# Kernel tuning notes

Measured on AMD Instinct MI355X. Metric: run time of the kernel, lower is better.

Reference implementation:

```python
import jax, jax.numpy as jnp
import numpy as np

B, S, DM = 2, 2048, 1024
H, HD = 16, 64  # heads, head_dims = dims // heads
SCALE = HD ** -0.5


def softmax_one(x):
    # softmax with +1 in the denominator: exp(x_i) / (1 + sum_j exp(x_j))
    # stable form: shift by m = max(max(x), 0)
    m = jnp.maximum(jnp.max(x, axis=-1, keepdims=True), 0.0)
    e = jnp.exp(x - m)
    return e / (jnp.exp(-m) + jnp.sum(e, axis=-1, keepdims=True))


def setup_inputs() -> dict:
    key = jax.random.key(0)
    ks = jax.random.split(key, 11)
    init = lambda k, shape, fan_in: jax.random.uniform(k, shape, jnp.float32, -1.0, 1.0) * (fan_in ** -0.5)
    return {
        "query": jax.random.normal(ks[0], (B, S, DM), jnp.float32),
        "key": jax.random.normal(ks[1], (B, S, DM), jnp.float32),
        "value": jax.random.normal(ks[2], (B, S, DM), jnp.float32),
        "Wq": init(ks[3], (H * HD, DM), DM), "bq": init(ks[4], (H * HD,), DM),
        "Wk": init(ks[5], (H * HD, DM), DM), "bk": init(ks[6], (H * HD,), DM),
        "Wv": init(ks[7], (H * HD, DM), DM), "bv": init(ks[8], (H * HD,), DM),
        "Wo": init(ks[9], (DM, H * HD), H * HD), "bo": init(ks[10], (DM,), H * HD),
    }


def _proj(x, W, b):
    # [B,S,DM] -> [B,H,S,HD]
    y = x @ W.T + b
    return y.reshape(B, S, H, HD).transpose(0, 2, 1, 3)


def reference(query, key, value, Wq, bq, Wk, bk, Wv, bv, Wo, bo):
    Q = _proj(query, Wq, bq)
    K = _proj(key, Wk, bk)
    V = _proj(value, Wv, bv)
    scores = jnp.einsum("bhqd,bhkd->bhqk", Q, K) * SCALE  # [B,H,S,S]
    attn = softmax_one(scores)
    out = jnp.einsum("bhqk,bhkd->bhqd", attn, V)  # [B,H,S,HD]
    out = out.transpose(0, 2, 1, 3).reshape(B, S, H * HD)
    return out @ Wo.T + bo
```

## Files before the change

kernel.cpp:

```cpp
#include <hip/hip_runtime.h>

#define B_ 2
#define S_ 2048
#define DM_ 1024
#define H_ 16
#define HD_ 64
#define SCALE_ 0.125f

typedef __bf16 bf16;
typedef __attribute__((ext_vector_type(4))) __bf16 bf16x4;
typedef __attribute__((ext_vector_type(8))) __bf16 bf16x8;
typedef __attribute__((ext_vector_type(4))) float f32x4;

#define MFMA16(a, b, c) __builtin_amdgcn_mfma_f32_16x16x32_bf16((a), (b), (c), 0, 0, 0)

__device__ __forceinline__ void async16(const bf16* g, bf16* l) {
  __builtin_amdgcn_global_load_lds(
      (const __attribute__((address_space(1))) void*)g,
      (__attribute__((address_space(3))) void*)l, 16, 0, 0);
}

__global__ __launch_bounds__(256) void convert_kernel(
    const float* __restrict__ q, const float* __restrict__ k,
    const float* __restrict__ v, const float* __restrict__ wq,
    const float* __restrict__ wk, const float* __restrict__ wv,
    const float* __restrict__ wo, bf16* __restrict__ dst) {
  size_t idx = ((size_t)blockIdx.x * 256 + threadIdx.x) * 8;
  const float* src;
  size_t off;
  if (idx < 4194304) { src = q; off = idx; }
  else if (idx < 8388608) { src = k; off = idx - 4194304; }
  else if (idx < 12582912) { src = v; off = idx - 8388608; }
  else if (idx < 13631488) { src = wq; off = idx - 12582912; }
  else if (idx < 14680064) { src = wk; off = idx - 13631488; }
  else if (idx < 15728640) { src = wv; off = idx - 14680064; }
  else { src = wo; off = idx - 15728640; }
  float4 a = *(const float4*)(src + off);
  float4 b = *(const float4*)(src + off + 4);
  bf16x8 o;
  o[0] = (bf16)a.x; o[1] = (bf16)a.y; o[2] = (bf16)a.z; o[3] = (bf16)a.w;
  o[4] = (bf16)b.x; o[5] = (bf16)b.y; o[6] = (bf16)b.z; o[7] = (bf16)b.w;
  *(bf16x8*)(dst + idx) = o;
}

template <int MODE, typename OutT>
__device__ __forceinline__ void gemm_body(const bf16* A, const bf16* W,
                                          const float* bias, OutT* C,
                                          float scale) {
  constexpr int K = 1024, N = 1024;
  __shared__ __align__(16) bf16 As[128 * 32];
  __shared__ __align__(16) bf16 Bs[128 * 32];
  const int t = threadIdx.x;
  const int lane = t & 63, wave = t >> 6;
  const int quad = lane >> 4, l16 = lane & 15;
  const int m0 = blockIdx.y * 128, n0 = blockIdx.x * 128;
  const int wm = (wave >> 1) * 64, wn = (wave & 1) * 64;

  const f32x4 zero = {0.f, 0.f, 0.f, 0.f};
  f32x4 acc[4][4];
  for (int i = 0; i < 4; i++)
    for (int j = 0; j < 4; j++) acc[i][j] = zero;

  for (int k0 = 0; k0 < K; k0 += 32) {
    for (int i = 0; i < 2; ++i) {
      int c = i * 256 + t;
      int row = c >> 2, kc = (c & 3) * 8;
      async16(A + (size_t)(m0 + row) * K + k0 + kc, As + c * 8);
      async16(W + (size_t)(n0 + row) * K + k0 + kc, Bs + c * 8);
    }
    __syncthreads();

    bf16x8 af[4], bfr[4];
    for (int mb = 0; mb < 4; mb++) {
      af[mb] = *(const bf16x8*)(As + (wm + mb * 16 + l16) * 32 + quad * 8);
      bfr[mb] = *(const bf16x8*)(Bs + (wn + mb * 16 + l16) * 32 + quad * 8);
    }
    for (int mb = 0; mb < 4; mb++)
      for (int nb = 0; nb < 4; nb++)
        acc[mb][nb] = MFMA16(af[mb], bfr[nb], acc[mb][nb]);
    __syncthreads();
  }

  if constexpr (MODE == 2) {
    __shared__ __align__(16) bf16 Ct[128 * 136];
    for (int nb = 0; nb < 4; nb++) {
      int cl = wn + nb * 16 + l16;
      float bv = bias[n0 + cl] * scale;
      for (int mb = 0; mb < 4; mb++) {
        int rowb = wm + mb * 16 + quad * 4;
        bf16x4 v;
        for (int r = 0; r < 4; r++)
          v[r] = (bf16)(acc[mb][nb][r] * scale + bv);
        *(bf16x4*)(Ct + cl * 136 + rowb) = v;
      }
    }
    __syncthreads();
    int c = t >> 1, half = t & 1;
    int colg = n0 + c;
    int hh = colg >> 6, dd = colg & 63;
    int bb = m0 >> 11, s0 = m0 & (S_ - 1);
    bf16* dst = C + (((size_t)(bb * H_ + hh)) * HD_ + dd) * S_ + s0 + half * 64;
    const bf16* srcr = Ct + c * 136 + half * 64;
    for (int j = 0; j < 8; ++j)
      *(bf16x8*)(dst + j * 8) = *(const bf16x8*)(srcr + j * 8);
  } else {
    for (int nb = 0; nb < 4; nb++) {
      int col = n0 + wn + nb * 16 + l16;
      float bv = bias[col] * scale;
      for (int mb = 0; mb < 4; mb++) {
        int rowb = m0 + wm + mb * 16 + quad * 4;
        for (int r = 0; r < 4; r++) {
          int row = rowb + r;
          float o = acc[mb][nb][r] * scale + bv;
          if (MODE == 0) {
            C[(size_t)row * N + col] = (OutT)o;
          } else {
            int bb = row >> 11, s = row & (S_ - 1);
            int h = col >> 6, d = col & 63;
            C[(((size_t)(bb * H_ + h)) * S_ + s) * HD_ + d] = (OutT)o;
          }
        }
      }
    }
  }
}

__global__ __launch_bounds__(256) void qkv_proj_kernel(
    const bf16* Xc, const float* bq, const float* bk, const float* bv,
    bf16* Qo, bf16* Ko, bf16* Vo) {
  int z = blockIdx.z;
  const bf16* A = Xc + (size_t)z * 4194304;
  const bf16* W = Xc + 12582912 + (size_t)z * 1048576;
  if (z == 0)
    gemm_body<1, bf16>(A, W, bq, Qo, SCALE_);
  else if (z == 1)
    gemm_body<1, bf16>(A, W, bk, Ko, 1.0f);
  else
    gemm_body<2, bf16>(A, W, bv, Vo, 1.0f);
}

__global__ __launch_bounds__(256) void out_proj_kernel(const bf16* A,
                                                       const bf16* W,
                                                       const float* bias,
                                                       float* C) {
  gemm_body<0, float>(A, W, bias, C, 1.0f);
}

__global__ __launch_bounds__(256) void attn_kernel(const bf16* __restrict__ Q,
                                                   const bf16* __restrict__ Kg,
                                                   const bf16* __restrict__ VTg,
                                                   bf16* __restrict__ O) {
  __shared__ __align__(16) bf16 Ks[128 * 64];
  __shared__ __align__(16) bf16 Vt[64 * 128];
  __shared__ __align__(16) bf16 Ps[4 * 32 * 136];
  const int t = threadIdx.x;
  const int lane = t & 63, wave = t >> 6;
  const int quad = lane >> 4, l16 = lane & 15;
  const int q0 = blockIdx.x * 128;
  const int h = blockIdx.y, b = blockIdx.z;
  const size_t base = ((size_t)(b * H_ + h)) * S_ * HD_;
  const bf16* Qp = Q + base;
  const bf16* Kp = Kg + base;
  const bf16* Vp = VTg + base;

  bf16x8 aq[2][2];
  for (int s = 0; s < 2; s++) {
    const bf16* qr = Qp + (size_t)(q0 + wave * 32 + s * 16 + l16) * HD_;
    aq[s][0] = *(const bf16x8*)(qr + quad * 8);
    aq[s][1] = *(const bf16x8*)(qr + 32 + quad * 8);
  }

  const f32x4 zero = {0.f, 0.f, 0.f, 0.f};
  f32x4 oc[2][4];
  for (int s = 0; s < 2; s++)
    for (int d = 0; d < 4; d++) oc[s][d] = zero;
  float rs[2] = {0.f, 0.f};

  bf16* Pw = Ps + wave * (32 * 136);

  for (int kv0 = 0; kv0 < S_; kv0 += 128) {
    for (int i = 0; i < 4; ++i) {
      int c = i * 256 + t;
      int row = c >> 3, g = c & 7;
      async16(Kp + (size_t)(kv0 + row) * HD_ + (g ^ (row & 7)) * 8, Ks + c * 8);
    }
    for (int i = 0; i < 4; ++i) {
      int c = i * 256 + t;
      int d = c >> 4, g = c & 15;
      async16(Vp + (size_t)d * S_ + kv0 + (g ^ (d & 15)) * 8, Vt + c * 8);
    }
    __syncthreads();

    f32x4 sc[2][8];
    for (int s = 0; s < 2; s++)
      for (int nb = 0; nb < 8; nb++) sc[s][nb] = zero;
    for (int ks = 0; ks < 2; ks++) {
      for (int nb = 0; nb < 8; nb++) {
        int row = nb * 16 + l16;
        int slot = (ks * 4 + quad) ^ (row & 7);
        bf16x8 kf = *(const bf16x8*)(Ks + row * 64 + slot * 8);
        sc[0][nb] = MFMA16(kf, aq[0][ks], sc[0][nb]);
        sc[1][nb] = MFMA16(kf, aq[1][ks], sc[1][nb]);
      }
    }

    for (int s = 0; s < 2; s++) {
      bf16* prow = Pw + (s * 16 + l16) * 136 + quad * 4;
      for (int nb = 0; nb < 8; nb++) {
        float p0 = __expf(sc[s][nb][0]);
        float p1 = __expf(sc[s][nb][1]);
        float p2 = __expf(sc[s][nb][2]);
        float p3 = __expf(sc[s][nb][3]);
        rs[s] += (p0 + p1) + (p2 + p3);
        bf16x4 pv = {(bf16)p0, (bf16)p1, (bf16)p2, (bf16)p3};
        *(bf16x4*)(prow + nb * 16) = pv;
      }
    }

    for (int ks = 0; ks < 4; ks++) {
      bf16x8 ap0 = *(const bf16x8*)(Pw + l16 * 136 + ks * 32 + quad * 8);
      bf16x8 ap1 = *(const bf16x8*)(Pw + (16 + l16) * 136 + ks * 32 + quad * 8);
      for (int db = 0; db < 4; db++) {
        int row = db * 16 + l16;
        int slot = (ks * 4 + quad) ^ (row & 15);
        bf16x8 vf = *(const bf16x8*)(Vt + row * 128 + slot * 8);
        oc[0][db] = MFMA16(ap0, vf, oc[0][db]);
        oc[1][db] = MFMA16(ap1, vf, oc[1][db]);
      }
    }
    __syncthreads();
  }

  for (int s = 0; s < 2; s++) {
    float rtot = rs[s];
    rtot += __shfl_xor(rtot, 16);
    rtot += __shfl_xor(rtot, 32);
    float l_all = 1.f + rtot;
    for (int r = 0; r < 4; r++) {
      float inv = 1.f / __shfl(l_all, quad * 4 + r);
      int qrow = q0 + wave * 32 + s * 16 + quad * 4 + r;
      size_t orow = ((size_t)(b * S_ + qrow) * H_ + h) * HD_;
      for (int db = 0; db < 4; db++)
        O[orow + db * 16 + l16] = (bf16)(oc[s][db][r] * inv);
    }
  }
}

extern "C" void kernel_launch(void* const* d_in, const int* in_sizes, int n_in,
                              void* d_out, int out_size, void* d_ws,
                              size_t ws_size, hipStream_t stream) {
  const float* query = (const float*)d_in[0];
  const float* key = (const float*)d_in[1];
  const float* value = (const float*)d_in[2];
  const float* bq = (const float*)d_in[4];
  const float* bk = (const float*)d_in[6];
  const float* bv = (const float*)d_in[8];
  const float* bo = (const float*)d_in[10];
  float* out = (float*)d_out;

  bf16* Xc = (bf16*)d_ws;
  bf16* Qw = Xc + 16777216;
  const size_t SZ = (size_t)B_ * H_ * S_ * HD_;
  bf16* Kw = Qw + SZ;
  bf16* Vw = Kw + SZ;
  bf16* Ow = Vw + SZ;

  convert_kernel<<<8192, 256, 0, stream>>>(query, key, value,
                                           (const float*)d_in[3],
                                           (const float*)d_in[5],
                                           (const float*)d_in[7],
                                           (const float*)d_in[9], Xc);
  qkv_proj_kernel<<<dim3(8, 32, 3), 256, 0, stream>>>(Xc, bq, bk, bv, Qw, Kw,
                                                      Vw);
  attn_kernel<<<dim3(S_ / 128, H_, B_), 256, 0, stream>>>(Qw, Kw, Vw, Ow);
  out_proj_kernel<<<dim3(8, 32), 256, 0, stream>>>(Ow, Xc + 15728640, bo, out);
}
```

Measured before the change: 245.3 us.

## Halve attention and out-proj tile sizes to launch more blocks

The attention kernel now gives each block 64 query rows (16 per wave) instead of 128, on a flat 1024-block grid ordered so blocks sharing a batch-head are spread across the grid. The output projection gets its own kernel with 64x128 tiles and one 16-row MFMA strip per wave, doubling its grid to 512 blocks. The goal is better CU occupancy on a chip with many CUs, where the old grids of 512 and 256 blocks left compute idle. The cost is that K/V tiles are reloaded from global or L2 twice as often, and each wave does less MFMA work per LDS fragment load.

Measured after the change: 258.8 us. 5.5% more time.

```diff
diff --git a/kernel.cpp b/kernel.cpp
--- a/kernel.cpp
+++ b/kernel.cpp
@@ -43,11 +43,11 @@
   *(bf16x8*)(dst + idx) = o;
 }
 
-template <int MODE, typename OutT>
+template <int MODE>
 __device__ __forceinline__ void gemm_body(const bf16* A, const bf16* W,
-                                          const float* bias, OutT* C,
+                                          const float* bias, bf16* C,
                                           float scale) {
-  constexpr int K = 1024, N = 1024;
+  constexpr int K = 1024;
   __shared__ __align__(16) bf16 As[128 * 32];
   __shared__ __align__(16) bf16 Bs[128 * 32];
   const int t = threadIdx.x;
@@ -112,13 +112,9 @@
         for (int r = 0; r < 4; r++) {
           int row = rowb + r;
           float o = acc[mb][nb][r] * scale + bv;
-          if (MODE == 0) {
-            C[(size_t)row * N + col] = (OutT)o;
-          } else {
-            int bb = row >> 11, s = row & (S_ - 1);
-            int h = col >> 6, d = col & 63;
-            C[(((size_t)(bb * H_ + h)) * S_ + s) * HD_ + d] = (OutT)o;
-          }
+          int bb = row >> 11, s = row & (S_ - 1);
+          int h = col >> 6, d = col & 63;
+          C[(((size_t)(bb * H_ + h)) * S_ + s) * HD_ + d] = (bf16)o;
         }
       }
     }
@@ -132,18 +128,56 @@
   const bf16* A = Xc + (size_t)z * 4194304;
   const bf16* W = Xc + 12582912 + (size_t)z * 1048576;
   if (z == 0)
-    gemm_body<1, bf16>(A, W, bq, Qo, SCALE_);
+    gemm_body<1>(A, W, bq, Qo, SCALE_);
   else if (z == 1)
-    gemm_body<1, bf16>(A, W, bk, Ko, 1.0f);
+    gemm_body<1>(A, W, bk, Ko, 1.0f);
   else
-    gemm_body<2, bf16>(A, W, bv, Vo, 1.0f);
+    gemm_body<2>(A, W, bv, Vo, 1.0f);
 }
 
 __global__ __launch_bounds__(256) void out_proj_kernel(const bf16* A,
                                                        const bf16* W,
                                                        const float* bias,
                                                        float* C) {
-  gemm_body<0, float>(A, W, bias, C, 1.0f);
+  constexpr int K = 1024, N = 1024;
+  __shared__ __align__(16) bf16 As[64 * 32];
+  __shared__ __align__(16) bf16 Bs[128 * 32];
+  const int t = threadIdx.x;
+  const int lane = t & 63, wave = t >> 6;
+  const int quad = lane >> 4, l16 = lane & 15;
+  const int m0 = blockIdx.y * 64, n0 = blockIdx.x * 128;
+
+  const f32x4 zero = {0.f, 0.f, 0.f, 0.f};
+  f32x4 acc[8];
+  for (int i = 0; i < 8; i++) acc[i] = zero;
+
+  for (int k0 = 0; k0 < K; k0 += 32) {
+    {
+      int row = t >> 2, kc = (t & 3) * 8;
+      async16(A + (size_t)(m0 + row) * K + k0 + kc, As + t * 8);
+    }
+    for (int i = 0; i < 2; ++i) {
+      int c = i * 256 + t;
+      int row = c >> 2, kc = (c & 3) * 8;
+      async16(W + (size_t)(n0 + row) * K + k0 + kc, Bs + c * 8);
+    }
+    __syncthreads();
+
+    bf16x8 af = *(const bf16x8*)(As + (wave * 16 + l16) * 32 + quad * 8);
+    for (int nb = 0; nb < 8; nb++) {
+      bf16x8 bfr = *(const bf16x8*)(Bs + (nb * 16 + l16) * 32 + quad * 8);
+      acc[nb] = MFMA16(af, bfr, acc[nb]);
+    }
+    __syncthreads();
+  }
+
+  for (int nb = 0; nb < 8; nb++) {
+    int col = n0 + nb * 16 + l16;
+    float bv = bias[col];
+    int rowb = m0 + wave * 16 + quad * 4;
+    for (int r = 0; r < 4; r++)
+      C[(size_t)(rowb + r) * N + col] = acc[nb][r] + bv;
+  }
 }
 
 __global__ __launch_bounds__(256) void attn_kernel(const bf16* __restrict__ Q,
@@ -152,31 +186,32 @@
                                                    bf16* __restrict__ O) {
   __shared__ __align__(16) bf16 Ks[128 * 64];
   __shared__ __align__(16) bf16 Vt[64 * 128];
-  __shared__ __align__(16) bf16 Ps[4 * 32 * 136];
+  __shared__ __align__(16) bf16 Ps[4 * 16 * 136];
   const int t = threadIdx.x;
   const int lane = t & 63, wave = t >> 6;
   const int quad = lane >> 4, l16 = lane & 15;
-  const int q0 = blockIdx.x * 128;
-  const int h = blockIdx.y, b = blockIdx.z;
+  const int id = blockIdx.x;
+  const int bh = id & 31;
+  const int q0 = (id >> 5) * 64;
+  const int b = bh >> 4, h = bh & 15;
   const size_t base = ((size_t)(b * H_ + h)) * S_ * HD_;
   const bf16* Qp = Q + base;
   const bf16* Kp = Kg + base;
   const bf16* Vp = VTg + base;
 
-  bf16x8 aq[2][2];
-  for (int s = 0; s < 2; s++) {
-    const bf16* qr = Qp + (size_t)(q0 + wave * 32 + s * 16 + l16) * HD_;
-    aq[s][0] = *(const bf16x8*)(qr + quad * 8);
-    aq[s][1] = *(const bf16x8*)(qr + 32 + quad * 8);
+  bf16x8 aq0, aq1;
+  {
+    const bf16* qr = Qp + (size_t)(q0 + wave * 16 + l16) * HD_;
+    aq0 = *(const bf16x8*)(qr + quad * 8);
+    aq1 = *(const bf16x8*)(qr + 32 + quad * 8);
   }
 
   const f32x4 zero = {0.f, 0.f, 0.f, 0.f};
-  f32x4 oc[2][4];
-  for (int s = 0; s < 2; s++)
-    for (int d = 0; d < 4; d++) oc[s][d] = zero;
-  float rs[2] = {0.f, 0.f};
-
-  bf16* Pw = Ps + wave * (32 * 136);
+  f32x4 oc[4];
+  for (int d = 0; d < 4; d++) oc[d] = zero;
+  float rs = 0.f;
+
+  bf16* Pw = Ps + wave * (16 * 136);
 
   for (int kv0 = 0; kv0 < S_; kv0 += 128) {
     for (int i = 0; i < 4; ++i) {
@@ -191,58 +226,51 @@
     }
     __syncthreads();
 
-    f32x4 sc[2][8];
-    for (int s = 0; s < 2; s++)
-      for (int nb = 0; nb < 8; nb++) sc[s][nb] = zero;
+    f32x4 sc[8];
+    for (int nb = 0; nb < 8; nb++) sc[nb] = zero;
     for (int ks = 0; ks < 2; ks++) {
+      bf16x8 qf = ks ? aq1 : aq0;
       for (int nb = 0; nb < 8; nb++) {
         int row = nb * 16 + l16;
         int slot = (ks * 4 + quad) ^ (row & 7);
         bf16x8 kf = *(const bf16x8*)(Ks + row * 64 + slot * 8);
-        sc[0][nb] = MFMA16(kf, aq[0][ks], sc[0][nb]);
-        sc[1][nb] = MFMA16(kf, aq[1][ks], sc[1][nb]);
+        sc[nb] = MFMA16(kf, qf, sc[nb]);
       }
     }
 
-    for (int s = 0; s < 2; s++) {
-      bf16* prow = Pw + (s * 16 + l16) * 136 + quad * 4;
-      for (int nb = 0; nb < 8; nb++) {
-        float p0 = __expf(sc[s][nb][0]);
-        float p1 = __expf(sc[s][nb][1]);
-        float p2 = __expf(sc[s][nb][2]);
-        float p3 = __expf(sc[s][nb][3]);
-        rs[s] += (p0 + p1) + (p2 + p3);
-        bf16x4 pv = {(bf16)p0, (bf16)p1, (bf16)p2, (bf16)p3};
-        *(bf16x4*)(prow + nb * 16) = pv;
-      }
+    bf16* prow = Pw + l16 * 136 + quad * 4;
+    for (int nb = 0; nb < 8; nb++) {
+      float p0 = __expf(sc[nb][0]);
+      float p1 = __expf(sc[nb][1]);
+      float p2 = __expf(sc[nb][2]);
+      float p3 = __expf(sc[nb][3]);
+      rs += (p0 + p1) + (p2 + p3);
+      bf16x4 pv = {(bf16)p0, (bf16)p1, (bf16)p2, (bf16)p3};
+      *(bf16x4*)(prow + nb * 16) = pv;
     }
 
     for (int ks = 0; ks < 4; ks++) {
-      bf16x8 ap0 = *(const bf16x8*)(Pw + l16 * 136 + ks * 32 + quad * 8);
-      bf16x8 ap1 = *(const bf16x8*)(Pw + (16 + l16) * 136 + ks * 32 + quad * 8);
+      bf16x8 ap = *(const bf16x8*)(Pw + l16 * 136 + ks * 32 + quad * 8);
       for (int db = 0; db < 4; db++) {
         int row = db * 16 + l16;
         int slot = (ks * 4 + quad) ^ (row & 15);
         bf16x8 vf = *(const bf16x8*)(Vt + row * 128 + slot * 8);
-        oc[0][db] = MFMA16(ap0, vf, oc[0][db]);
-        oc[1][db] = MFMA16(ap1, vf, oc[1][db]);
+        oc[db] = MFMA16(ap, vf, oc[db]);
       }
     }
     __syncthreads();
   }
 
-  for (int s = 0; s < 2; s++) {
-    float rtot = rs[s];
-    rtot += __shfl_xor(rtot, 16);
-    rtot += __shfl_xor(rtot, 32);
-    float l_all = 1.f + rtot;
-    for (int r = 0; r < 4; r++) {
-      float inv = 1.f / __shfl(l_all, quad * 4 + r);
-      int qrow = q0 + wave * 32 + s * 16 + quad * 4 + r;
-      size_t orow = ((size_t)(b * S_ + qrow) * H_ + h) * HD_;
-      for (int db = 0; db < 4; db++)
-        O[orow + db * 16 + l16] = (bf16)(oc[s][db][r] * inv);
-    }
+  float rtot = rs;
+  rtot += __shfl_xor(rtot, 16);
+  rtot += __shfl_xor(rtot, 32);
+  float l_all = 1.f + rtot;
+  for (int r = 0; r < 4; r++) {
+    float inv = 1.f / __shfl(l_all, quad * 4 + r);
+    int qrow = q0 + wave * 16 + quad * 4 + r;
+    size_t orow = ((size_t)(b * S_ + qrow) * H_ + h) * HD_;
+    for (int db = 0; db < 4; db++)
+      O[orow + db * 16 + l16] = (bf16)(oc[db][r] * inv);
   }
 }
 
@@ -272,6 +300,6 @@
                                            (const float*)d_in[9], Xc);
   qkv_proj_kernel<<<dim3(8, 32, 3), 256, 0, stream>>>(Xc, bq, bk, bv, Qw, Kw,
                                                       Vw);
-  attn_kernel<<<dim3(S_ / 128, H_, B_), 256, 0, stream>>>(Qw, Kw, Vw, Ow);
-  out_proj_kernel<<<dim3(8, 32), 256, 0, stream>>>(Ow, Xc + 15728640, bo, out);
-}
+  attn_kernel<<<1024, 256, 0, stream>>>(Qw, Kw, Vw, Ow);
+  out_proj_kernel<<<dim3(8, 64), 256, 0, stream>>>(Ow, Xc + 15728640, bo, out);
+}
```
